# Kernel tuning notes

Hardware: AMD Instinct MI355X
Metric: run time of the kernel (lower is better)

The kernel has to match this reference:

```python
import jax, jax.numpy as jnp
import numpy as np

B, N, DIM, HEADS, DIM_HEAD = 2, 2048, 1024, 16, 64
INNER = HEADS * DIM_HEAD
LN_EPS = 1e-5


def setup_inputs() -> dict:
    key = jax.random.key(0)
    k1, k2, k3 = jax.random.split(key, 3)
    x = jax.random.normal(k1, (B, N, DIM), dtype=jnp.float32)
    ln_w = jnp.ones((DIM,), dtype=jnp.float32)
    ln_b = jnp.zeros((DIM,), dtype=jnp.float32)
    w_qkv = jax.random.normal(k2, (DIM, 3 * INNER), dtype=jnp.float32) * (DIM ** -0.5)
    w_out = jax.random.normal(k3, (INNER, DIM), dtype=jnp.float32) * (INNER ** -0.5)
    return {"x": x, "ln_w": ln_w, "ln_b": ln_b, "w_qkv": w_qkv, "w_out": w_out}


def reference(x, ln_w, ln_b, w_qkv, w_out):
    scale = DIM_HEAD ** -0.5
    # LayerNorm over last dim
    mu = jnp.mean(x, axis=-1, keepdims=True)
    var = jnp.var(x, axis=-1, keepdims=True)
    xn = (x - mu) / jnp.sqrt(var + LN_EPS) * ln_w + ln_b
    # qkv projection, split, reshape to b h n d
    qkv = xn @ w_qkv  # [B, N, 3*INNER]
    q, k, v = jnp.split(qkv, 3, axis=-1)
    def to_heads(t):
        return t.reshape(B, N, HEADS, DIM_HEAD).transpose(0, 2, 1, 3)
    q, k, v = to_heads(q) * scale, to_heads(k), to_heads(v)
    # scores + causal mask (triu with offset 1 masked)
    sim = jnp.einsum('bhid,bhjd->bhij', q, k)  # [B, H, N, N]
    causal_mask = jnp.triu(jnp.ones((N, N), dtype=bool), k=1)
    sim = jnp.where(causal_mask, -jnp.finfo(sim.dtype).max, sim)
    attn = jax.nn.softmax(sim, axis=-1)
    out = jnp.einsum('bhij,bhjd->bhid', attn, v)  # [B, H, N, D]
    out = out.transpose(0, 2, 1, 3).reshape(B, N, INNER)
    return out @ w_out
```

## Files before the change

kernel.cpp:

```cpp
#include <hip/hip_runtime.h>
#include <stdint.h>

#define BATCH 2
#define NSEQ  2048
#define DIMC  1024
#define NHEAD 16
#define DHEAD 64
#define QKVN  3072
#define MROWS 4096

typedef __attribute__((ext_vector_type(8))) unsigned short u16x8;
typedef __attribute__((ext_vector_type(4))) unsigned short u16x4;
typedef __attribute__((ext_vector_type(8))) short          bf16x8;
typedef __attribute__((ext_vector_type(4))) short          s16x4;
typedef __attribute__((ext_vector_type(4))) float          f32x4;

#define F32_PROBE 0x3F800000u
#define QSCALE 0.18033688f

__device__ __forceinline__ float b2f(unsigned short u) {
  union { unsigned int i; float f; } c; c.i = ((unsigned int)u) << 16; return c.f;
}
__device__ __forceinline__ unsigned short f2b(float f) {
  unsigned int u = __float_as_uint(f);
  return (unsigned short)((u + 0x7fffu + ((u >> 16) & 1u)) >> 16);
}
__device__ __forceinline__ float fast_exp2(float x) {
  return __builtin_amdgcn_exp2f(x);
}
__device__ __forceinline__ void async16(const unsigned short* g, unsigned short* s) {
  __builtin_amdgcn_global_load_lds(
      (const __attribute__((address_space(1))) unsigned int*)g,
      (__attribute__((address_space(3))) unsigned int*)s, 16, 0, 0);
}
__device__ __forceinline__ f32x4 mfma_k16(s16x4 a, s16x4 b, f32x4 c) {
#if __has_builtin(__builtin_amdgcn_mfma_f32_16x16x16bf16_1k)
  return __builtin_amdgcn_mfma_f32_16x16x16bf16_1k(a, b, c, 0, 0, 0);
#else
  asm("v_mfma_f32_16x16x16_bf16 %0, %1, %2, %0" : "+v"(c) : "v"(a), "v"(b));
  return c;
#endif
}

__device__ __forceinline__ void tr_tile(const void* __restrict__ in,
                                        unsigned short* __restrict__ out,
                                        int R, int C, int r0, int c0, bool f32,
                                        int t, unsigned short (*tile)[33],
                                        int scale_below) {
  int tx = t & 31, ty = t >> 5;
  float sc = (c0 < scale_below) ? QSCALE : 1.0f;
  if (f32) {
    #pragma unroll
    for (int i = 0; i < 32; i += 8)
      tile[ty + i][tx] = f2b(((const float*)in)[(size_t)(r0 + ty + i) * C + c0 + tx] * sc);
  } else {
    #pragma unroll
    for (int i = 0; i < 32; i += 8)
      tile[ty + i][tx] = f2b(b2f(((const unsigned short*)in)[(size_t)(r0 + ty + i) * C + c0 + tx]) * sc);
  }
  __syncthreads();
  #pragma unroll
  for (int i = 0; i < 32; i += 8)
    out[(size_t)(c0 + ty + i) * R + r0 + tx] = tile[tx][ty + i];
}

__global__ __launch_bounds__(256) void prep_kernel(const void* __restrict__ x,
                                                   const void* __restrict__ w,
                                                   const void* __restrict__ bb,
                                                   unsigned short* __restrict__ xn,
                                                   const void* __restrict__ w_qkv,
                                                   unsigned short* __restrict__ wqkvT,
                                                   const void* __restrict__ w_out,
                                                   unsigned short* __restrict__ woutT,
                                                   const unsigned int* __restrict__ probe) {
  __shared__ unsigned short tile[32][33];
  __shared__ float red[8];
  bool f32 = (*probe == F32_PROBE);
  int bid = blockIdx.x, t = threadIdx.x;

  if (bid < MROWS) {
    int row = bid;
    float v0, v1, v2, v3, w0, w1, w2, w3, bb0, bb1, bb2, bb3;
    if (f32) {
      const float* xr = (const float*)x + (size_t)row * DIMC;
      float4 xv = *(const float4*)(xr + t * 4);
      v0 = xv.x; v1 = xv.y; v2 = xv.z; v3 = xv.w;
      float4 wv = *(const float4*)((const float*)w + t * 4);
      w0 = wv.x; w1 = wv.y; w2 = wv.z; w3 = wv.w;
      float4 bv = *(const float4*)((const float*)bb + t * 4);
      bb0 = bv.x; bb1 = bv.y; bb2 = bv.z; bb3 = bv.w;
    } else {
      const unsigned short* xr = (const unsigned short*)x + (size_t)row * DIMC;
      u16x4 xv = *(const u16x4*)(xr + t * 4);
      v0 = b2f(xv[0]); v1 = b2f(xv[1]); v2 = b2f(xv[2]); v3 = b2f(xv[3]);
      u16x4 wv = *(const u16x4*)((const unsigned short*)w + t * 4);
      w0 = b2f(wv[0]); w1 = b2f(wv[1]); w2 = b2f(wv[2]); w3 = b2f(wv[3]);
      u16x4 bv = *(const u16x4*)((const unsigned short*)bb + t * 4);
      bb0 = b2f(bv[0]); bb1 = b2f(bv[1]); bb2 = b2f(bv[2]); bb3 = b2f(bv[3]);
    }
    float s = v0 + v1 + v2 + v3;
    float q = v0 * v0 + v1 * v1 + v2 * v2 + v3 * v3;
    #pragma unroll
    for (int off = 1; off < 64; off <<= 1) { s += __shfl_xor(s, off); q += __shfl_xor(q, off); }
    int wv_ = t >> 6;
    if ((t & 63) == 0) { red[wv_] = s; red[4 + wv_] = q; }
    __syncthreads();
    s = red[0] + red[1] + red[2] + red[3];
    q = red[4] + red[5] + red[6] + red[7];
    float mu  = s * (1.0f / DIMC);
    float var = q * (1.0f / DIMC) - mu * mu;
    float rstd = rsqrtf(var + 1e-5f);
    u16x4 o;
    o[0] = f2b((v0 - mu) * rstd * w0 + bb0);
    o[1] = f2b((v1 - mu) * rstd * w1 + bb1);
    o[2] = f2b((v2 - mu) * rstd * w2 + bb2);
    o[3] = f2b((v3 - mu) * rstd * w3 + bb3);
    *(u16x4*)(xn + (size_t)row * DIMC + t * 4) = o;
  } else if (bid < MROWS + 3072) {
    int tid = bid - MROWS;
    tr_tile(w_qkv, wqkvT, DIMC, QKVN, (tid / 96) * 32, (tid % 96) * 32, f32, t, tile, 1024);
  } else {
    int tid = bid - (MROWS + 3072);
    tr_tile(w_out, woutT, DIMC, DIMC, (tid >> 5) * 32, (tid & 31) * 32, f32, t, tile, 0);
  }
}

__global__ __launch_bounds__(256) void transpose_kernel(const void* __restrict__ in,
                                                        unsigned short* __restrict__ out,
                                                        int R, int C,
                                                        const unsigned int* __restrict__ probe) {
  __shared__ unsigned short tile[32][33];
  bool f32 = (*probe == F32_PROBE);
  int t = threadIdx.x;
  tr_tile(in, out, R, C, blockIdx.y * 32, blockIdx.x * 32, f32, t, tile, 0);
}

__device__ __forceinline__ void ldA8(bf16x8 (&dst)[8], const unsigned short* base,
                                     int off, int ch0, int ch1) {
  #pragma unroll
  for (int mi = 0; mi < 4; ++mi) {
    dst[mi * 2 + 0] = *(const bf16x8*)&base[off + mi * 1024 + ch0];
    dst[mi * 2 + 1] = *(const bf16x8*)&base[off + mi * 1024 + ch1];
  }
}
__device__ __forceinline__ void ldB3(bf16x8 (&dst)[3], const unsigned short* base,
                                     int off, int ch) {
  #pragma unroll
  for (int ni = 0; ni < 3; ++ni)
    dst[ni] = *(const bf16x8*)&base[off + ni * 1024 + ch];
}
__device__ __forceinline__ void mfma12(f32x4 (&acc)[4][6], const bf16x8 (&a)[8],
                                       const bf16x8 (&b)[3], int C, int kh) {
  #pragma unroll
  for (int mi = 0; mi < 4; ++mi)
    #pragma unroll
    for (int ni = 0; ni < 3; ++ni)
      acc[mi][C * 3 + ni] = __builtin_amdgcn_mfma_f32_16x16x32_bf16(
          a[mi * 2 + kh], b[ni], acc[mi][C * 3 + ni], 0, 0, 0);
}

#define SB    asm volatile("s_barrier" ::: "memory")
#define WVM4  asm volatile("s_waitcnt vmcnt(4)" ::: "memory")
#define WLG0  asm volatile("s_waitcnt lgkmcnt(0)" ::: "memory")
#define PRIO1 __builtin_amdgcn_s_setprio(1)
#define PRIO0 __builtin_amdgcn_s_setprio(0)
#define STG(gp, g, k0, sb) async16((gp) + (size_t)(g) * 65536 + (k0), (sb) + (g) * 4096 + t8)

__global__ __launch_bounds__(512) void gemm1_8p(const unsigned short* __restrict__ A,
                                                const unsigned short* __restrict__ Bt,
                                                unsigned short* __restrict__ C,
                                                unsigned short* __restrict__ vt_out) {
  __shared__ unsigned short lds[57344];
  unsigned short* A0b = lds;
  unsigned short* A1b = lds + 16384;
  unsigned short* B0b = lds + 32768;
  unsigned short* B1b = lds + 45056;

  int t = threadIdx.x;
  int lane = t & 63, wv = t >> 6;
  int l16 = lane & 15, quad = lane >> 4;
  int wr = wv >> 1, wc = wv & 1;

  int bid = blockIdx.x;
  int xcd = bid & 7, rr = bid >> 3;
  int bx = (xcd & 3) * 4 + (rr >> 3);
  int by = (xcd >> 2) * 8 + (rr & 7);
  int bm = bx * 256, bn = by * 192;

  int rl = t >> 3;
  int sc8 = (((t & 7) ^ (rl & 7)) << 3);
  int t8 = t * 8;
  const unsigned short* Ag = A  + (size_t)(bm + rl) * 1024 + sc8;
  const unsigned short* Bg = Bt + (size_t)(bn + rl) * 1024 + sc8;

  int aoff = (wr * 64 + l16) * 64;
  int boff = (wc * 96 + l16) * 64;
  int ch0 = ((quad ^ (l16 & 7)) << 3);
  int ch1 = (((quad + 4) ^ (l16 & 7)) << 3);

  f32x4 acc[4][6] = {};
  bf16x8 ar[8], bcE[3], bcO[3];

  STG(Ag, 0, 0, A0b); STG(Ag, 1, 0, A0b); STG(Ag, 2, 0, A0b); STG(Ag, 3, 0, A0b);
  STG(Bg, 0, 0, B0b); STG(Bg, 1, 0, B0b); STG(Bg, 2, 0, B0b);
  STG(Ag, 0, 64, A1b); STG(Ag, 1, 64, A1b); STG(Ag, 2, 64, A1b); STG(Ag, 3, 64, A1b);
  WVM4;
  SB;

  for (int i = 0; i < 8; ++i) {
    const int k_b1 = (2 * i + 1) * 64;
    const int k_n0 = ((2 * i + 2) & 15) * 64;
    const int k_n1 = ((2 * i + 3) & 15) * 64;

    ldA8(ar, A0b, aoff, ch0, ch1);
    ldB3(bcE, B0b, boff, ch0);
    STG(Bg, 0, k_b1, B1b); STG(Bg, 1, k_b1, B1b);
    SB; WLG0; PRIO1; mfma12(acc, ar, bcE, 0, 0); PRIO0; SB;
    ldB3(bcO, B0b, boff + 3072, ch0);
    STG(Bg, 2, k_b1, B1b);
    SB; WLG0; PRIO1; mfma12(acc, ar, bcO, 1, 0); PRIO0; SB;
    ldB3(bcE, B0b, boff, ch1);
    STG(Ag, 0, k_n0, A0b); STG(Ag, 1, k_n0, A0b);
    SB; WLG0; PRIO1; mfma12(acc, ar, bcE, 0, 1); PRIO0; SB;
    ldB3(bcO, B0b, boff + 3072, ch1);
    STG(Ag, 2, k_n0, A0b); STG(Ag, 3, k_n0, A0b);
    WVM4;
    SB; WLG0; PRIO1; mfma12(acc, ar, bcO, 1, 1); PRIO0; SB;

    ldA8(ar, A1b, aoff, ch0, ch1);
    ldB3(bcE, B1b, boff, ch0);
    STG(Bg, 0, k_n0, B0b); STG(Bg, 1, k_n0, B0b);
    SB; WLG0; PRIO1; mfma12(acc, ar, bcE, 0, 0); PRIO0; SB;
    ldB3(bcO, B1b, boff + 3072, ch0);
    STG(Bg, 2, k_n0, B0b);
    SB; WLG0; PRIO1; mfma12(acc, ar, bcO, 1, 0); PRIO0; SB;
    ldB3(bcE, B1b, boff, ch1);
    STG(Ag, 0, k_n1, A1b); STG(Ag, 1, k_n1, A1b);
    SB; WLG0; PRIO1; mfma12(acc, ar, bcE, 0, 1); PRIO0; SB;
    ldB3(bcO, B1b, boff + 3072, ch1);
    STG(Ag, 2, k_n1, A1b); STG(Ag, 3, k_n1, A1b);
    WVM4;
    SB; WLG0; PRIO1; mfma12(acc, ar, bcO, 1, 1); PRIO0; SB;
  }

  #pragma unroll
  for (int rf = 0; rf < 4; ++rf)
    #pragma unroll
    for (int cf = 0; cf < 6; ++cf) {
      int gr0 = bm + wr * 64 + rf * 16 + quad * 4;
      int gc  = bn + wc * 96 + cf * 16 + l16;
      if (gc >= 2048) {
        int hh = (gc >> 6) & 15;
        int dd = gc & 63;
        int bb2 = gr0 >> 11;
        int n0  = gr0 & 2047;
        u16x4 pk;
        #pragma unroll
        for (int r = 0; r < 4; r++) pk[r] = f2b(acc[rf][cf][r]);
        *(u16x4*)&vt_out[(((size_t)(bb2 * 16 + hh) * 64 + dd) << 11) + n0] = pk;
      } else {
        #pragma unroll
        for (int r = 0; r < 4; r++)
          C[(size_t)(gr0 + r) * QKVN + gc] = f2b(acc[rf][cf][r]);
      }
    }
}

__device__ __forceinline__ void ld4(bf16x8 (&dst)[4], const unsigned short* base,
                                    int off, int ch0, int ch1) {
  #pragma unroll
  for (int m = 0; m < 2; ++m) {
    dst[m * 2 + 0] = *(const bf16x8*)&base[off + m * 1024 + ch0];
    dst[m * 2 + 1] = *(const bf16x8*)&base[off + m * 1024 + ch1];
  }
}
__device__ __forceinline__ void mfma8(f32x4 (&acc)[4][4], const bf16x8 (&a)[4],
                                      const bf16x8 (&b)[4], int R, int C) {
  #pragma unroll
  for (int kh = 0; kh < 2; ++kh)
    #pragma unroll
    for (int m = 0; m < 2; ++m)
      #pragma unroll
      for (int n = 0; n < 2; ++n)
        acc[R * 2 + m][C * 2 + n] = __builtin_amdgcn_mfma_f32_16x16x32_bf16(
            a[m * 2 + kh], b[n * 2 + kh], acc[R * 2 + m][C * 2 + n], 0, 0, 0);
}
#define STG2A(g, k0, sb) async16(Ag + (size_t)(g) * 32 * QKVN + (k0), (sb) + (g) * 2048 + t8)
#define STG2B(g, k0, sb) async16(Bg + (size_t)(g) * 32 * 1024 + (k0), (sb) + (g) * 2048 + t8)

__global__ __launch_bounds__(256) void gemm2_8p(const unsigned short* __restrict__ A,
                                                const unsigned short* __restrict__ Bt,
                                                void* __restrict__ Cv,
                                                const unsigned int* __restrict__ probe) {
  __shared__ unsigned short lds[32768];
  unsigned short* A0b = lds;
  unsigned short* A1b = lds + 8192;
  unsigned short* B0b = lds + 16384;
  unsigned short* B1b = lds + 24576;

  int t = threadIdx.x;
  int lane = t & 63, wv = t >> 6;
  int l16 = lane & 15, quad = lane >> 4;
  int wr = wv >> 1, wc = wv & 1;

  int bid = blockIdx.x;
  int xcd = bid & 7, rr = bid >> 3;
  int bx = xcd * 4 + (rr >> 3);
  int by = rr & 7;
  int bm = bx * 128, bn = by * 128;

  int rl = t >> 3;
  int sc8 = (((t & 7) ^ (rl & 7)) << 3);
  int t8 = t * 8;
  const unsigned short* Ag = A  + (size_t)(bm + rl) * QKVN + sc8;
  const unsigned short* Bg = Bt + (size_t)(bn + rl) * 1024 + sc8;

  int aoff = (wr * 64 + l16) * 64;
  int boff = (wc * 64 + l16) * 64;
  int ch0 = ((quad ^ (l16 & 7)) << 3);
  int ch1 = (((quad + 4) ^ (l16 & 7)) << 3);

  f32x4 acc[4][4] = {};
  bf16x8 arE[4], arO[4], bcE[4], bcO[4];

  STG2A(0, 0, A0b); STG2A(1, 0, A0b); STG2A(2, 0, A0b); STG2A(3, 0, A0b);
  STG2B(0, 0, B0b); STG2B(1, 0, B0b); STG2B(2, 0, B0b); STG2B(3, 0, B0b);
  STG2A(0, 64, A1b); STG2A(1, 64, A1b); STG2A(2, 64, A1b); STG2A(3, 64, A1b);
  WVM4;
  SB;

  for (int i = 0; i < 8; ++i) {
    const int k_b1 = (2 * i + 1) * 64;
    const int k_n0 = ((2 * i + 2) & 15) * 64;
    const int k_n1 = ((2 * i + 3) & 15) * 64;

    ld4(arE, A0b, aoff, ch0, ch1);
    ld4(bcE, B0b, boff, ch0, ch1);
    STG2B(0, k_b1, B1b); STG2B(1, k_b1, B1b);
    SB; WLG0; PRIO1; mfma8(acc, arE, bcE, 0, 0); PRIO0; SB;
    ld4(arO, A0b, aoff + 2048, ch0, ch1);
    STG2B(2, k_b1, B1b); STG2B(3, k_b1, B1b);
    SB; WLG0; PRIO1; mfma8(acc, arO, bcE, 1, 0); PRIO0; SB;
    ld4(bcO, B0b, boff + 2048, ch0, ch1);
    STG2A(0, k_n0, A0b); STG2A(1, k_n0, A0b);
    SB; WLG0; PRIO1; mfma8(acc, arE, bcO, 0, 1); PRIO0; SB;
    STG2A(2, k_n0, A0b); STG2A(3, k_n0, A0b);
    WVM4;
    SB; PRIO1; mfma8(acc, arO, bcO, 1, 1); PRIO0; SB;

    ld4(arE, A1b, aoff, ch0, ch1);
    ld4(bcE, B1b, boff, ch0, ch1);
    STG2B(0, k_n0, B0b); STG2B(1, k_n0, B0b);
    SB; WLG0; PRIO1; mfma8(acc, arE, bcE, 0, 0); PRIO0; SB;
    ld4(arO, A1b, aoff + 2048, ch0, ch1);
    STG2B(2, k_n0, B0b); STG2B(3, k_n0, B0b);
    SB; WLG0; PRIO1; mfma8(acc, arO, bcE, 1, 0); PRIO0; SB;
    ld4(bcO, B1b, boff + 2048, ch0, ch1);
    STG2A(0, k_n1, A1b); STG2A(1, k_n1, A1b);
    SB; WLG0; PRIO1; mfma8(acc, arE, bcO, 0, 1); PRIO0; SB;
    STG2A(2, k_n1, A1b); STG2A(3, k_n1, A1b);
    WVM4;
    SB; PRIO1; mfma8(acc, arO, bcO, 1, 1); PRIO0; SB;
  }

  bool f32out = (*probe == F32_PROBE);
  #pragma unroll
  for (int rf = 0; rf < 4; ++rf)
    #pragma unroll
    for (int cf = 0; cf < 4; ++cf) {
      int gr0 = bm + wr * 64 + rf * 16 + quad * 4;
      int gc  = bn + wc * 64 + cf * 16 + l16;
      #pragma unroll
      for (int r = 0; r < 4; r++) {
        if (f32out) ((float*)Cv)[(size_t)(gr0 + r) * DIMC + gc] = acc[rf][cf][r];
        else ((unsigned short*)Cv)[(size_t)(gr0 + r) * DIMC + gc] = f2b(acc[rf][cf][r]);
      }
    }
}

__device__ __forceinline__ int swz(int row, int chunk) {
  return row * 64 + ((chunk ^ (row & 7)) << 3);
}
#define OSW(d, c) ((d) * 64 + ((((c)) ^ ((d) & 15)) << 2))

__global__ __launch_bounds__(256, 3) void attn_v7(unsigned short* __restrict__ qkv,
                                                  const unsigned short* __restrict__ vt) {
  __shared__ unsigned short lds[16384];

  int t = threadIdx.x;
  int lane = t & 63, w = t >> 6;
  int l16 = lane & 15, quad = lane >> 4;
  int id = blockIdx.x;
  int xcd = id & 7, jj = id >> 3;
  int bh = xcd + ((jj & 3) << 3);
  int qt = 31 - (jj >> 2);
  int b = bh >> 4, h = bh & 15;
  unsigned short* qbase = qkv + (size_t)(b * NSEQ) * QKVN + h * DHEAD;
  const unsigned short* kbase = qbase + 1024;
  const unsigned short* vtb = vt + (size_t)bh * DHEAD * NSEQ;

  int sr = t >> 3, sc = t & 7;
  int sw8 = ((sc ^ (sr & 7)) << 3);
  int q0 = qt * 64;

  bf16x8 bq0[4], bq1[4];
  #pragma unroll
  for (int qb = 0; qb < 4; qb++) {
    const unsigned short* qp = qbase + (size_t)(q0 + qb * 16 + l16) * QKVN + quad * 8;
    bq0[qb] = *(const bf16x8*)(qp);
    bq1[qb] = *(const bf16x8*)(qp + 32);
  }

  float l4[4] = {0.f, 0.f, 0.f, 0.f};
  f32x4 o[4][4] = {};

  async16(kbase + (size_t)sr * QKVN + sw8,              lds + t * 8);
  async16(kbase + (size_t)(sr + 32) * QKVN + sw8,       lds + 2048 + t * 8);
  async16(vtb + (size_t)sr * NSEQ + sw8,                lds + 8192 + t * 8);
  async16(vtb + (size_t)(sr + 32) * NSEQ + sw8,         lds + 8192 + 2048 + t * 8);
  __syncthreads();

  for (int jt = 0; jt <= qt; jt++) {
    const unsigned short* Kc = lds + (jt & 1) * 4096;
    const unsigned short* Vc = lds + 8192 + (jt & 1) * 4096;

    if (jt < qt) {
      int j0n = (jt + 1) * 64;
      unsigned short* Kn = lds + ((jt + 1) & 1) * 4096;
      unsigned short* Vn = lds + 8192 + ((jt + 1) & 1) * 4096;
      async16(kbase + (size_t)(j0n + sr) * QKVN + sw8,      Kn + t * 8);
      async16(kbase + (size_t)(j0n + sr + 32) * QKVN + sw8, Kn + 2048 + t * 8);
      async16(vtb + (size_t)sr * NSEQ + j0n + sw8,          Vn + t * 8);
      async16(vtb + (size_t)(sr + 32) * NSEQ + j0n + sw8,   Vn + 2048 + t * 8);
    }

    bf16x8 ak0 = *(const bf16x8*)&Kc[swz(w * 16 + l16, quad)];
    bf16x8 ak1 = *(const bf16x8*)&Kc[swz(w * 16 + l16, 4 + quad)];
    f32x4 sv[4];
    PRIO1;
    #pragma unroll
    for (int qb = 0; qb < 4; qb++) {
      f32x4 s = {-32.0f, -32.0f, -32.0f, -32.0f};
      s = __builtin_amdgcn_mfma_f32_16x16x32_bf16(ak0, bq0[qb], s, 0, 0, 0);
      s = __builtin_amdgcn_mfma_f32_16x16x32_bf16(ak1, bq1[qb], s, 0, 0, 0);
      sv[qb] = s;
    }
    PRIO0;

    s16x4 pa[4];
    #pragma unroll
    for (int qb = 0; qb < 4; qb++) {
      float p0 = fast_exp2(sv[qb][0]);
      float p1 = fast_exp2(sv[qb][1]);
      float p2 = fast_exp2(sv[qb][2]);
      float p3 = fast_exp2(sv[qb][3]);
      if (jt == qt) {
        int jl = w * 16 + quad * 4, ql = qb * 16 + l16;
        if (jl + 0 > ql) p0 = 0.f;
        if (jl + 1 > ql) p1 = 0.f;
        if (jl + 2 > ql) p2 = 0.f;
        if (jl + 3 > ql) p3 = 0.f;
      }
      l4[qb] += (p0 + p1) + (p2 + p3);
      union { unsigned int u[2]; s16x4 v; } cc;
      asm("v_cvt_pk_bf16_f32 %0, %1, %2" : "=v"(cc.u[0]) : "v"(p0), "v"(p1));
      asm("v_cvt_pk_bf16_f32 %0, %1, %2" : "=v"(cc.u[1]) : "v"(p2), "v"(p3));
      pa[qb] = cc.v;
    }

    PRIO1;
    #pragma unroll
    for (int db = 0; db < 4; db++) {
      u16x4 vb = *(const u16x4*)&Vc[swz(db * 16 + l16, 2 * w + (quad >> 1)) + (quad & 1) * 4];
      union { u16x4 u; s16x4 s; } vc; vc.u = vb;
      #pragma unroll
      for (int qb = 0; qb < 4; qb++)
        o[qb][db] = mfma_k16(pa[qb], vc.s, o[qb][db]);
    }
    PRIO0;

    if (jt < qt) __syncthreads();
  }

  #pragma unroll
  for (int qb = 0; qb < 4; qb++) {
    l4[qb] += __shfl_xor(l4[qb], 16);
    l4[qb] += __shfl_xor(l4[qb], 32);
  }
  __syncthreads();
  float* f = (float*)lds;
  if (quad == 0) {
    #pragma unroll
    for (int qb = 0; qb < 4; qb++) f[w * 64 + qb * 16 + l16] = l4[qb];
  }
  __syncthreads();
  #pragma unroll
  for (int qb = 0; qb < 4; qb++)
    l4[qb] = (f[qb * 16 + l16] + f[64 + qb * 16 + l16]) +
             (f[128 + qb * 16 + l16] + f[192 + qb * 16 + l16]);
  __syncthreads();

  float* r0 = f;
  float* r1 = f + 4096;
  if (w == 1 || w == 3) {
    float* rg = (w == 1) ? r0 : r1;
    #pragma unroll
    for (int qb = 0; qb < 4; qb++)
      #pragma unroll
      for (int db = 0; db < 4; db++)
        *(f32x4*)&rg[OSW(db * 16 + l16, qb * 4 + quad)] = o[qb][db];
  }
  __syncthreads();
  if (w == 0 || w == 2) {
    float* rg = (w == 0) ? r0 : r1;
    #pragma unroll
    for (int qb = 0; qb < 4; qb++)
      #pragma unroll
      for (int db = 0; db < 4; db++)
        o[qb][db] += *(const f32x4*)&rg[OSW(db * 16 + l16, qb * 4 + quad)];
  }
  __syncthreads();
  if (w == 2) {
    #pragma unroll
    for (int qb = 0; qb < 4; qb++)
      #pragma unroll
      for (int db = 0; db < 4; db++)
        *(f32x4*)&r0[OSW(db * 16 + l16, qb * 4 + quad)] = o[qb][db];
  }
  __syncthreads();
  if (w == 0) {
    #pragma unroll
    for (int qb = 0; qb < 4; qb++) {
      #pragma unroll
      for (int db = 0; db < 4; db++)
        o[qb][db] += *(const f32x4*)&r0[OSW(db * 16 + l16, qb * 4 + quad)];
      #pragma unroll
      for (int r = 0; r < 4; r++) {
        float lr = __shfl(l4[qb], (lane & 48) | (quad * 4 + r));
        float inv = 1.0f / lr;
        int row = q0 + qb * 16 + quad * 4 + r;
        #pragma unroll
        for (int db = 0; db < 4; db++)
          qbase[(size_t)row * QKVN + db * 16 + l16] = f2b(o[qb][db][r] * inv);
      }
    }
  }
}

extern "C" void kernel_launch(void* const* d_in, const int* in_sizes, int n_in,
                              void* d_out, int out_size, void* d_ws, size_t ws_size,
                              hipStream_t stream) {
  const void* x     = d_in[0];
  const void* ln_w  = d_in[1];
  const void* ln_b  = d_in[2];
  const void* w_qkv = d_in[3];
  const void* w_out = d_in[4];
  const unsigned int* probe = (const unsigned int*)d_in[1];

  unsigned short* wqkvT = (unsigned short*)d_ws;
  unsigned short* qkv   = wqkvT + (size_t)QKVN * DIMC;
  unsigned short* xn    = (unsigned short*)d_out;
  size_t base_e  = (size_t)QKVN * DIMC + (size_t)MROWS * QKVN;
  size_t vt_e    = (size_t)BATCH * NHEAD * DHEAD * NSEQ;
  size_t wout_e  = (size_t)DIMC * DIMC;
  bool fit_vt  = ws_size >= (base_e + vt_e) * 2;
  bool fit_all = ws_size >= (base_e + vt_e + wout_e) * 2;
  unsigned short* vtp   = fit_vt ? qkv + (size_t)MROWS * QKVN
                                 : ((unsigned short*)d_out) + ((size_t)4 * 1024 * 1024);
  unsigned short* woutT = fit_all ? vtp + vt_e : wqkvT;

  int prep_blocks = MROWS + 3072 + (fit_all ? 1024 : 0);
  prep_kernel<<<prep_blocks, 256, 0, stream>>>(x, ln_w, ln_b, xn, w_qkv, wqkvT,
                                               w_out, fit_all ? woutT : nullptr, probe);
  gemm1_8p<<<dim3(256), 512, 0, stream>>>(xn, wqkvT, qkv, vtp);
  if (!fit_all)
    transpose_kernel<<<dim3(DIMC / 32, DIMC / 32), 256, 0, stream>>>(w_out, woutT, DIMC, DIMC, probe);
  attn_v7<<<dim3(1024), 256, 0, stream>>>(qkv, vtp);
  gemm2_8p<<<dim3(256), 256, 0, stream>>>(qkv, woutT, d_out, probe);
}
```

Baseline: 164.3 us.

## Give each attention wave private K/V LDS slices and drop block barriers

Each wave now stages only the 16 K rows and matching V columns it consumes into its own LDS region, so the per-iteration __syncthreads is replaced by per-wave vmcnt waits. This removes block-wide barrier stalls in the causal attention inner loop and lets waves drift independently. It changes the LDS layout and swizzle for K and V. The wait relies on the async copies completing in order, and without a barrier the write-after-read safety on the double buffer depends on the wave's own program order.

```diff
diff --git a/kernel.cpp b/kernel.cpp
--- a/kernel.cpp
+++ b/kernel.cpp
@@ -161,6 +161,7 @@
 
 #define SB    asm volatile("s_barrier" ::: "memory")
 #define WVM4  asm volatile("s_waitcnt vmcnt(4)" ::: "memory")
+#define WVM0  asm volatile("s_waitcnt vmcnt(0)" ::: "memory")
 #define WLG0  asm volatile("s_waitcnt lgkmcnt(0)" ::: "memory")
 #define PRIO1 __builtin_amdgcn_s_setprio(1)
 #define PRIO0 __builtin_amdgcn_s_setprio(0)
@@ -378,12 +379,9 @@
     }
 }
 
-__device__ __forceinline__ int swz(int row, int chunk) {
-  return row * 64 + ((chunk ^ (row & 7)) << 3);
-}
 #define OSW(d, c) ((d) * 64 + ((((c)) ^ ((d) & 15)) << 2))
 
-__global__ __launch_bounds__(256, 3) void attn_v7(unsigned short* __restrict__ qkv,
+__global__ __launch_bounds__(256, 3) void attn_v8(unsigned short* __restrict__ qkv,
                                                   const unsigned short* __restrict__ vt) {
   __shared__ unsigned short lds[16384];
 
@@ -398,10 +396,22 @@
   unsigned short* qbase = qkv + (size_t)(b * NSEQ) * QKVN + h * DHEAD;
   const unsigned short* kbase = qbase + 1024;
   const unsigned short* vtb = vt + (size_t)bh * DHEAD * NSEQ;
-
-  int sr = t >> 3, sc = t & 7;
-  int sw8 = ((sc ^ (sr & 7)) << 3);
   int q0 = qt * 64;
+
+  unsigned short* wbase = lds + w * 4096;
+  int lane8 = lane * 8;
+  int kr = lane >> 3;
+  int kchunk = (lane & 7) ^ kr;
+  size_t kgo = (size_t)(w * 16 + kr) * QKVN + kchunk * 8;
+  int vd = lane >> 1;
+  int vh = (lane & 1) ^ ((vd >> 2) & 1);
+  size_t vgo = (size_t)vd * NSEQ + w * 16 + vh * 8;
+
+#define STAGE_V8(j0, Kb, Vb) do { \
+    async16(kbase + (size_t)(j0) * QKVN + kgo,       (Kb) + lane8);       \
+    async16(kbase + (size_t)((j0) + 8) * QKVN + kgo, (Kb) + 512 + lane8); \
+    async16(vtb + (size_t)(j0) + vgo,                (Vb) + lane8);       \
+    async16(vtb + (size_t)(j0) + 32 * NSEQ + vgo,    (Vb) + 512 + lane8); } while (0)
 
   bf16x8 bq0[4], bq1[4];
   #pragma unroll
@@ -414,28 +424,24 @@
   float l4[4] = {0.f, 0.f, 0.f, 0.f};
   f32x4 o[4][4] = {};
 
-  async16(kbase + (size_t)sr * QKVN + sw8,              lds + t * 8);
-  async16(kbase + (size_t)(sr + 32) * QKVN + sw8,       lds + 2048 + t * 8);
-  async16(vtb + (size_t)sr * NSEQ + sw8,                lds + 8192 + t * 8);
-  async16(vtb + (size_t)(sr + 32) * NSEQ + sw8,         lds + 8192 + 2048 + t * 8);
-  __syncthreads();
+  STAGE_V8(0, wbase, wbase + 2048);
 
   for (int jt = 0; jt <= qt; jt++) {
-    const unsigned short* Kc = lds + (jt & 1) * 4096;
-    const unsigned short* Vc = lds + 8192 + (jt & 1) * 4096;
+    unsigned short* Kb = wbase + (jt & 1) * 1024;
+    unsigned short* Vb = wbase + 2048 + (jt & 1) * 1024;
 
     if (jt < qt) {
       int j0n = (jt + 1) * 64;
-      unsigned short* Kn = lds + ((jt + 1) & 1) * 4096;
-      unsigned short* Vn = lds + 8192 + ((jt + 1) & 1) * 4096;
-      async16(kbase + (size_t)(j0n + sr) * QKVN + sw8,      Kn + t * 8);
-      async16(kbase + (size_t)(j0n + sr + 32) * QKVN + sw8, Kn + 2048 + t * 8);
-      async16(vtb + (size_t)sr * NSEQ + j0n + sw8,          Vn + t * 8);
-      async16(vtb + (size_t)(sr + 32) * NSEQ + j0n + sw8,   Vn + 2048 + t * 8);
-    }
-
-    bf16x8 ak0 = *(const bf16x8*)&Kc[swz(w * 16 + l16, quad)];
-    bf16x8 ak1 = *(const bf16x8*)&Kc[swz(w * 16 + l16, 4 + quad)];
+      unsigned short* Kn = wbase + ((jt + 1) & 1) * 1024;
+      unsigned short* Vn = wbase + 2048 + ((jt + 1) & 1) * 1024;
+      STAGE_V8(j0n, Kn, Vn);
+      WVM4;
+    } else {
+      WVM0;
+    }
+
+    bf16x8 ak0 = *(const bf16x8*)&Kb[l16 * 64 + ((quad ^ (l16 & 7)) << 3)];
+    bf16x8 ak1 = *(const bf16x8*)&Kb[l16 * 64 + (((quad + 4) ^ (l16 & 7)) << 3)];
     f32x4 sv[4];
     PRIO1;
     #pragma unroll
@@ -471,15 +477,15 @@
     PRIO1;
     #pragma unroll
     for (int db = 0; db < 4; db++) {
-      u16x4 vb = *(const u16x4*)&Vc[swz(db * 16 + l16, 2 * w + (quad >> 1)) + (quad & 1) * 4];
+      int d = db * 16 + l16;
+      int hh = (quad >> 1) ^ ((l16 >> 2) & 1);
+      u16x4 vb = *(const u16x4*)&Vb[d * 16 + hh * 8 + (quad & 1) * 4];
       union { u16x4 u; s16x4 s; } vc; vc.u = vb;
       #pragma unroll
       for (int qb = 0; qb < 4; qb++)
         o[qb][db] = mfma_k16(pa[qb], vc.s, o[qb][db]);
     }
     PRIO0;
-
-    if (jt < qt) __syncthreads();
   }
 
   #pragma unroll
@@ -575,6 +581,6 @@
   gemm1_8p<<<dim3(256), 512, 0, stream>>>(xn, wqkvT, qkv, vtp);
   if (!fit_all)
     transpose_kernel<<<dim3(DIMC / 32, DIMC / 32), 256, 0, stream>>>(w_out, woutT, DIMC, DIMC, probe);
-  attn_v7<<<dim3(1024), 256, 0, stream>>>(qkv, vtp);
+  attn_v8<<<dim3(1024), 256, 0, stream>>>(qkv, vtp);
   gemm2_8p<<<dim3(256), 256, 0, stream>>>(qkv, woutT, d_out, probe);
 }
```

Measured after the change: 163.3 us. About the same (-0.6%).

## Load K/V fragments directly into registers instead of staging through LDS

Applied to the files above, without the earlier changes.

The attention kernel stops staging each K and V^T tile through double-buffered shared memory with async copies and barriers. Each wave now loads only its own K and V fragments straight from global memory into registers, prefetching the next tile into registers while the current one is computed. This removes the LDS traffic and the per-iteration __syncthreads. In exchange it issues less coalesced global loads (4-element V reads), drops the cross-wave sharing of tiles, and raises register pressure, so launch bounds drop from 3 to 2 blocks per CU.

```diff
diff --git a/kernel.cpp b/kernel.cpp
--- a/kernel.cpp
+++ b/kernel.cpp
@@ -378,13 +378,10 @@
     }
 }
 
-__device__ __forceinline__ int swz(int row, int chunk) {
-  return row * 64 + ((chunk ^ (row & 7)) << 3);
-}
 #define OSW(d, c) ((d) * 64 + ((((c)) ^ ((d) & 15)) << 2))
 
-__global__ __launch_bounds__(256, 3) void attn_v7(unsigned short* __restrict__ qkv,
-                                                  const unsigned short* __restrict__ vt) {
+__global__ __launch_bounds__(256, 2) void attn_v10(unsigned short* __restrict__ qkv,
+                                                   const unsigned short* __restrict__ vt) {
   __shared__ unsigned short lds[16384];
 
   int t = threadIdx.x;
@@ -398,10 +395,10 @@
   unsigned short* qbase = qkv + (size_t)(b * NSEQ) * QKVN + h * DHEAD;
   const unsigned short* kbase = qbase + 1024;
   const unsigned short* vtb = vt + (size_t)bh * DHEAD * NSEQ;
-
-  int sr = t >> 3, sc = t & 7;
-  int sw8 = ((sc ^ (sr & 7)) << 3);
   int q0 = qt * 64;
+
+  const unsigned short* kp = kbase + (size_t)(w * 16 + l16) * QKVN + quad * 8;
+  const unsigned short* vp = vtb + (size_t)l16 * NSEQ + w * 16 + quad * 4;
 
   bf16x8 bq0[4], bq1[4];
   #pragma unroll
@@ -414,35 +411,33 @@
   float l4[4] = {0.f, 0.f, 0.f, 0.f};
   f32x4 o[4][4] = {};
 
-  async16(kbase + (size_t)sr * QKVN + sw8,              lds + t * 8);
-  async16(kbase + (size_t)(sr + 32) * QKVN + sw8,       lds + 2048 + t * 8);
-  async16(vtb + (size_t)sr * NSEQ + sw8,                lds + 8192 + t * 8);
-  async16(vtb + (size_t)(sr + 32) * NSEQ + sw8,         lds + 8192 + 2048 + t * 8);
-  __syncthreads();
+  bf16x8 ka0 = *(const bf16x8*)(kp);
+  bf16x8 ka1 = *(const bf16x8*)(kp + 32);
+  u16x4 va0 = *(const u16x4*)(vp);
+  u16x4 va1 = *(const u16x4*)(vp + 16 * NSEQ);
+  u16x4 va2 = *(const u16x4*)(vp + 32 * NSEQ);
+  u16x4 va3 = *(const u16x4*)(vp + 48 * NSEQ);
 
   for (int jt = 0; jt <= qt; jt++) {
-    const unsigned short* Kc = lds + (jt & 1) * 4096;
-    const unsigned short* Vc = lds + 8192 + (jt & 1) * 4096;
-
+    bf16x8 kn0, kn1; u16x4 vn0, vn1, vn2, vn3;
     if (jt < qt) {
+      size_t kjo = (size_t)(jt + 1) * 64 * QKVN;
       int j0n = (jt + 1) * 64;
-      unsigned short* Kn = lds + ((jt + 1) & 1) * 4096;
-      unsigned short* Vn = lds + 8192 + ((jt + 1) & 1) * 4096;
-      async16(kbase + (size_t)(j0n + sr) * QKVN + sw8,      Kn + t * 8);
-      async16(kbase + (size_t)(j0n + sr + 32) * QKVN + sw8, Kn + 2048 + t * 8);
-      async16(vtb + (size_t)sr * NSEQ + j0n + sw8,          Vn + t * 8);
-      async16(vtb + (size_t)(sr + 32) * NSEQ + j0n + sw8,   Vn + 2048 + t * 8);
-    }
-
-    bf16x8 ak0 = *(const bf16x8*)&Kc[swz(w * 16 + l16, quad)];
-    bf16x8 ak1 = *(const bf16x8*)&Kc[swz(w * 16 + l16, 4 + quad)];
+      kn0 = *(const bf16x8*)(kp + kjo);
+      kn1 = *(const bf16x8*)(kp + kjo + 32);
+      vn0 = *(const u16x4*)(vp + j0n);
+      vn1 = *(const u16x4*)(vp + 16 * NSEQ + j0n);
+      vn2 = *(const u16x4*)(vp + 32 * NSEQ + j0n);
+      vn3 = *(const u16x4*)(vp + 48 * NSEQ + j0n);
+    }
+
     f32x4 sv[4];
     PRIO1;
     #pragma unroll
     for (int qb = 0; qb < 4; qb++) {
       f32x4 s = {-32.0f, -32.0f, -32.0f, -32.0f};
-      s = __builtin_amdgcn_mfma_f32_16x16x32_bf16(ak0, bq0[qb], s, 0, 0, 0);
-      s = __builtin_amdgcn_mfma_f32_16x16x32_bf16(ak1, bq1[qb], s, 0, 0, 0);
+      s = __builtin_amdgcn_mfma_f32_16x16x32_bf16(ka0, bq0[qb], s, 0, 0, 0);
+      s = __builtin_amdgcn_mfma_f32_16x16x32_bf16(ka1, bq1[qb], s, 0, 0, 0);
       sv[qb] = s;
     }
     PRIO0;
@@ -469,17 +464,23 @@
     }
 
     PRIO1;
-    #pragma unroll
-    for (int db = 0; db < 4; db++) {
-      u16x4 vb = *(const u16x4*)&Vc[swz(db * 16 + l16, 2 * w + (quad >> 1)) + (quad & 1) * 4];
-      union { u16x4 u; s16x4 s; } vc; vc.u = vb;
-      #pragma unroll
-      for (int qb = 0; qb < 4; qb++)
-        o[qb][db] = mfma_k16(pa[qb], vc.s, o[qb][db]);
+    {
+      union { u16x4 u; s16x4 s; } v0c, v1c, v2c, v3c;
+      v0c.u = va0; v1c.u = va1; v2c.u = va2; v3c.u = va3;
+      #pragma unroll
+      for (int qb = 0; qb < 4; qb++) {
+        o[qb][0] = mfma_k16(pa[qb], v0c.s, o[qb][0]);
+        o[qb][1] = mfma_k16(pa[qb], v1c.s, o[qb][1]);
+        o[qb][2] = mfma_k16(pa[qb], v2c.s, o[qb][2]);
+        o[qb][3] = mfma_k16(pa[qb], v3c.s, o[qb][3]);
+      }
     }
     PRIO0;
 
-    if (jt < qt) __syncthreads();
+    if (jt < qt) {
+      ka0 = kn0; ka1 = kn1;
+      va0 = vn0; va1 = vn1; va2 = vn2; va3 = vn3;
+    }
   }
 
   #pragma unroll
@@ -575,6 +576,6 @@
   gemm1_8p<<<dim3(256), 512, 0, stream>>>(xn, wqkvT, qkv, vtp);
   if (!fit_all)
     transpose_kernel<<<dim3(DIMC / 32, DIMC / 32), 256, 0, stream>>>(w_out, woutT, DIMC, DIMC, probe);
-  attn_v7<<<dim3(1024), 256, 0, stream>>>(qkv, vtp);
+  attn_v10<<<dim3(1024), 256, 0, stream>>>(qkv, vtp);
   gemm2_8p<<<dim3(256), 256, 0, stream>>>(qkv, woutT, d_out, probe);
 }
```

Measured after the change: 187.6 us. +14.2%, slower.
